# Kernel tuning notes

Hardware: AMD Instinct MI355X
Metric: run time of the kernel (lower is better)

## Reference

```python
import jax, jax.numpy as jnp
import numpy as np

N_NODES = 50000
N_EDGES = 800000
D_IN = 64
D_OUT = 64


def setup_inputs() -> dict:
    key = jax.random.key(0)
    ks = jax.random.split(key, 5)
    feat = jax.random.normal(ks[0], (N_NODES, D_IN), dtype=jnp.float32)
    src = jax.random.randint(ks[1], (N_EDGES,), 0, N_NODES, dtype=jnp.int64)
    dst = jax.random.randint(ks[2], (N_EDGES,), 0, N_NODES, dtype=jnp.int64)
    # Xavier-uniform-ish scale for weights
    lim = float(np.sqrt(6.0 / (D_IN + D_OUT)) * np.sqrt(2.0))
    W_neigh = jax.random.uniform(ks[3], (D_OUT, D_IN), dtype=jnp.float32, minval=-lim, maxval=lim)
    W_self = jax.random.uniform(ks[4], (D_OUT, D_IN), dtype=jnp.float32, minval=-lim, maxval=lim)
    b_self = jnp.zeros((D_OUT,), dtype=jnp.float32)
    return {"feat": feat, "src": src, "dst": dst,
            "W_neigh": W_neigh, "W_self": W_self, "b_self": b_self}


def reference(feat, src, dst, W_neigh, W_self, b_self):
    # srcdata = fc_neigh(feat_src)  -> [N, D_OUT]
    srcdata = feat @ W_neigh.T
    # A_div.T @ srcdata == mean of transformed source feats over in-edges per dst.
    # deg[j] = A.sum(0)[j]; column scaling by 1/deg then transpose-SpMM.
    agg = jax.ops.segment_sum(srcdata[src], dst, num_segments=N_NODES)  # [N, D_OUT]
    deg = jax.ops.segment_sum(jnp.ones_like(dst, dtype=srcdata.dtype), dst,
                              num_segments=N_NODES)  # [N]
    # Zero-degree columns stay zero in the sparse product (no stored nonzeros).
    dstdata = jnp.where(deg[:, None] > 0, agg / jnp.maximum(deg, 1.0)[:, None], 0.0)
    # rst = fc_self(feat_dst) + dstdata ; feat_dst = feat[:N_dst] = feat (square A)
    return feat @ W_self.T + b_self + dstdata
```

## Files before the change

### kernel.cpp

```cpp
#include <hip/hip_runtime.h>

#define N_NODES 50000
#define N_EDGES 800000
#define D 64
#define RB 128
#define NBUCK 391
#define NFEATBLK 3125
#define GN 64
#define NCHUNK 196
#define CHUNK 4096
#define SUBCAP 40
#define SCAP 3072
#define ALD 68

typedef __attribute__((ext_vector_type(8))) __bf16 bf16x8;
typedef __attribute__((ext_vector_type(4))) float f32x4;
typedef __attribute__((ext_vector_type(2))) float f32x2;

__device__ inline unsigned f2bf(float f) {
    unsigned b = __builtin_bit_cast(unsigned, f);
    b += 0x7fffu + ((b >> 16) & 1u);
    return b >> 16;
}

__device__ inline void acc16(float* acc, uint4 v) {
    f32x2 a;
    a = __builtin_amdgcn_cvt_pk_f32_fp8((int)v.x, false); acc[0]  += a.x; acc[1]  += a.y;
    a = __builtin_amdgcn_cvt_pk_f32_fp8((int)v.x, true);  acc[2]  += a.x; acc[3]  += a.y;
    a = __builtin_amdgcn_cvt_pk_f32_fp8((int)v.y, false); acc[4]  += a.x; acc[5]  += a.y;
    a = __builtin_amdgcn_cvt_pk_f32_fp8((int)v.y, true);  acc[6]  += a.x; acc[7]  += a.y;
    a = __builtin_amdgcn_cvt_pk_f32_fp8((int)v.z, false); acc[8]  += a.x; acc[9]  += a.y;
    a = __builtin_amdgcn_cvt_pk_f32_fp8((int)v.z, true);  acc[10] += a.x; acc[11] += a.y;
    a = __builtin_amdgcn_cvt_pk_f32_fp8((int)v.w, false); acc[12] += a.x; acc[13] += a.y;
    a = __builtin_amdgcn_cvt_pk_f32_fp8((int)v.w, true);  acc[14] += a.x; acc[15] += a.y;
}

__global__ __launch_bounds__(256) void prep_scatter_kernel(
        const float* __restrict__ feat, const float* __restrict__ Wn, const float* __restrict__ Ws,
        const int* __restrict__ src, const int* __restrict__ dst,
        unsigned* __restrict__ fq,
        unsigned short* __restrict__ wnb, unsigned short* __restrict__ wsb,
        unsigned int* __restrict__ ebuf, unsigned char* __restrict__ cntArr) {
    __shared__ int cntB[NBUCK];
    int b = blockIdx.x;
    int t = threadIdx.x;
    if (b < NCHUNK) {
        for (int i = t; i < NBUCK; i += 256) cntB[i] = 0;
        __syncthreads();
        int e0 = b * CHUNK;
#pragma unroll
        for (int k = 0; k < 16; ++k) {
            int e = e0 + k * 256 + t;
            if (e < N_EDGES) {
                int dv = dst[e];
                int bk = dv >> 7;
                int slot = atomicAdd(&cntB[bk], 1);
                if (slot < SUBCAP)
                    ebuf[((size_t)bk * NCHUNK + b) * SUBCAP + slot] =
                        (unsigned)src[e] | ((unsigned)(dv & (RB - 1)) << 16);
            }
        }
        __syncthreads();
        for (int i = t; i < NBUCK; i += 256) {
            int c = cntB[i];
            cntArr[(size_t)b * NBUCK + i] = (unsigned char)(c < SUBCAP ? c : SUBCAP);
        }
    } else if (b < NCHUNK + NFEATBLK) {
        int i = (b - NCHUNK) * 256 + t;
        float4 v = ((const float4*)feat)[i];
        int q = __builtin_amdgcn_cvt_pk_fp8_f32(v.x, v.y, 0, false);
        q = __builtin_amdgcn_cvt_pk_fp8_f32(v.z, v.w, q, true);
        fq[i] = (unsigned)q;
    } else {
        for (int i = t; i < D * D; i += 256) {
            wnb[i] = (unsigned short)f2bf(Wn[i]);
            wsb[i] = (unsigned short)f2bf(Ws[i]);
        }
    }
}

__global__ __launch_bounds__(256) void gather_mfma_kernel(
        const float* __restrict__ feat, const unsigned char* __restrict__ fq,
        const unsigned int* __restrict__ ebuf, const unsigned char* __restrict__ cntArr,
        const unsigned short* __restrict__ wsb, const unsigned short* __restrict__ wnb,
        const float* __restrict__ bias, float* __restrict__ out) {
    __shared__ int cnt[RB];
    __shared__ int cur[RB];
    __shared__ unsigned short sorted[SCAP];
    __shared__ float agg[GN * ALD];
    int t = threadIdx.x;
    int bk = blockIdx.x >> 1;
    int half = blockIdx.x & 1;
    if (t < RB) cnt[t] = 0;
    __syncthreads();
    int cc = 0;
    const unsigned int* slab = ebuf + ((size_t)bk * NCHUNK + t) * SUBCAP;
    if (t < NCHUNK) cc = cntArr[(size_t)t * NBUCK + bk];
    for (int j = 0; j < cc; j += 4) {
        uint4 v = *(const uint4*)(slab + j);
        atomicAdd(&cnt[(v.x >> 16) & (RB - 1)], 1);
        if (j + 1 < cc) atomicAdd(&cnt[(v.y >> 16) & (RB - 1)], 1);
        if (j + 2 < cc) atomicAdd(&cnt[(v.z >> 16) & (RB - 1)], 1);
        if (j + 3 < cc) atomicAdd(&cnt[(v.w >> 16) & (RB - 1)], 1);
    }
    __syncthreads();
    int c = (t < RB) ? cnt[t] : 0;
    if (t < RB) cur[t] = c;
    __syncthreads();
    for (int d = 1; d < RB; d <<= 1) {
        int v = (t < RB && t >= d) ? cur[t - d] : 0;
        __syncthreads();
        if (t < RB) cur[t] += v;
        __syncthreads();
    }
    if (t < RB) cur[t] -= c;
    __syncthreads();
    for (int j = 0; j < cc; j += 4) {
        uint4 v = *(const uint4*)(slab + j);
        int p;
        p = atomicAdd(&cur[(v.x >> 16) & (RB - 1)], 1);
        if (p < SCAP) sorted[p] = (unsigned short)(v.x & 0xFFFFu);
        if (j + 1 < cc) { p = atomicAdd(&cur[(v.y >> 16) & (RB - 1)], 1); if (p < SCAP) sorted[p] = (unsigned short)(v.y & 0xFFFFu); }
        if (j + 2 < cc) { p = atomicAdd(&cur[(v.z >> 16) & (RB - 1)], 1); if (p < SCAP) sorted[p] = (unsigned short)(v.z & 0xFFFFu); }
        if (j + 3 < cc) { p = atomicAdd(&cur[(v.w >> 16) & (RB - 1)], 1); if (p < SCAP) sorted[p] = (unsigned short)(v.w & 0xFFFFu); }
    }
    __syncthreads();
    int ns = t >> 2, p = t & 3;
    int dl = half * GN + ns;
    int dg = cnt[dl];
    int start = cur[dl] - dg;
    float acc[16];
#pragma unroll
    for (int j = 0; j < 16; ++j) acc[j] = 0.f;
    const unsigned char* fqp = fq + p * 16;
    int i = 0;
    for (; i + 4 <= dg; i += 4) {
        int id0 = sorted[start + i + 0];
        int id1 = sorted[start + i + 1];
        int id2 = sorted[start + i + 2];
        int id3 = sorted[start + i + 3];
        uint4 v0 = *(const uint4*)(fqp + (size_t)id0 * D);
        uint4 v1 = *(const uint4*)(fqp + (size_t)id1 * D);
        uint4 v2 = *(const uint4*)(fqp + (size_t)id2 * D);
        uint4 v3 = *(const uint4*)(fqp + (size_t)id3 * D);
        acc16(acc, v0); acc16(acc, v1); acc16(acc, v2); acc16(acc, v3);
    }
    for (; i < dg; ++i) {
        int id = sorted[start + i];
        uint4 v = *(const uint4*)(fqp + (size_t)id * D);
        acc16(acc, v);
    }
    float inv = (dg > 0) ? 1.0f / (float)dg : 0.f;
#pragma unroll
    for (int j = 0; j < 16; j += 4) {
        float4 o = make_float4(acc[j] * inv, acc[j + 1] * inv, acc[j + 2] * inv, acc[j + 3] * inv);
        *(float4*)(&agg[ns * ALD + p * 16 + j]) = o;
    }
    __syncthreads();
    int r0 = blockIdx.x * GN;
    int w = t >> 6, lane = t & 63;
    int m = lane & 15, quad = lane >> 4;
    int row = r0 + 16 * w + m;
    int rowA = row < N_NODES ? row : N_NODES - 1;
    const float* fr = feat + (size_t)rowA * D + quad * 8;
    float4 f0 = *(const float4*)(fr + 0);
    float4 f1 = *(const float4*)(fr + 4);
    float4 f2 = *(const float4*)(fr + 32);
    float4 f3 = *(const float4*)(fr + 36);
    bf16x8 aS0, aS1, aA0, aA1;
    aS0[0] = (__bf16)f0.x; aS0[1] = (__bf16)f0.y; aS0[2] = (__bf16)f0.z; aS0[3] = (__bf16)f0.w;
    aS0[4] = (__bf16)f1.x; aS0[5] = (__bf16)f1.y; aS0[6] = (__bf16)f1.z; aS0[7] = (__bf16)f1.w;
    aS1[0] = (__bf16)f2.x; aS1[1] = (__bf16)f2.y; aS1[2] = (__bf16)f2.z; aS1[3] = (__bf16)f2.w;
    aS1[4] = (__bf16)f3.x; aS1[5] = (__bf16)f3.y; aS1[6] = (__bf16)f3.z; aS1[7] = (__bf16)f3.w;
#pragma unroll
    for (int j = 0; j < 8; ++j) {
        aA0[j] = (__bf16)agg[(16 * w + m) * ALD + 0  + quad * 8 + j];
        aA1[j] = (__bf16)agg[(16 * w + m) * ALD + 32 + quad * 8 + j];
    }
#pragma unroll
    for (int tt = 0; tt < 4; ++tt) {
        int nn = 16 * tt + m;
        bf16x8 bS0 = *(const bf16x8*)(wsb + (size_t)nn * D + 0  + quad * 8);
        bf16x8 bS1 = *(const bf16x8*)(wsb + (size_t)nn * D + 32 + quad * 8);
        bf16x8 bN0 = *(const bf16x8*)(wnb + (size_t)nn * D + 0  + quad * 8);
        bf16x8 bN1 = *(const bf16x8*)(wnb + (size_t)nn * D + 32 + quad * 8);
        f32x4 cc4 = {0.f, 0.f, 0.f, 0.f};
        cc4 = __builtin_amdgcn_mfma_f32_16x16x32_bf16(aS0, bS0, cc4, 0, 0, 0);
        cc4 = __builtin_amdgcn_mfma_f32_16x16x32_bf16(aS1, bS1, cc4, 0, 0, 0);
        cc4 = __builtin_amdgcn_mfma_f32_16x16x32_bf16(aA0, bN0, cc4, 0, 0, 0);
        cc4 = __builtin_amdgcn_mfma_f32_16x16x32_bf16(aA1, bN1, cc4, 0, 0, 0);
        float bv = bias[16 * tt + m];
#pragma unroll
        for (int reg = 0; reg < 4; ++reg) {
            int orow = r0 + 16 * w + quad * 4 + reg;
            if (orow < N_NODES)
                out[(size_t)orow * D + 16 * tt + m] = cc4[reg] + bv;
        }
    }
}

extern "C" void kernel_launch(void* const* d_in, const int* in_sizes, int n_in,
                              void* d_out, int out_size, void* d_ws, size_t ws_size,
                              hipStream_t stream) {
    const float* feat  = (const float*)d_in[0];
    const int*   src   = (const int*)d_in[1];
    const int*   dst   = (const int*)d_in[2];
    const float* Wn    = (const float*)d_in[3];
    const float* Wself = (const float*)d_in[4];
    const float* bself = (const float*)d_in[5];
    float* out = (float*)d_out;

    unsigned*       featq = (unsigned*)d_ws;
    unsigned short* wnb   = (unsigned short*)(featq + (size_t)N_NODES * D / 4);
    unsigned short* wsb   = wnb + D * D;
    unsigned int*   ebuf  = (unsigned int*)(wsb + D * D);
    unsigned char*  cntArr = (unsigned char*)(ebuf + (size_t)NBUCK * NCHUNK * SUBCAP);

    prep_scatter_kernel<<<NCHUNK + NFEATBLK + 1, 256, 0, stream>>>(
        feat, Wn, Wself, src, dst, featq, wnb, wsb, ebuf, cntArr);
    gather_mfma_kernel<<<2 * NBUCK, 256, 0, stream>>>(
        feat, (const unsigned char*)featq, ebuf, cntArr, wsb, wnb, bself, out);
}
```

Measured before the change: 114.1 us.

## Split gather blocks into quarter-buckets and two-way split each node's edge list

The gather kernel now launches four blocks per 128-node bucket instead of two, with each block handling 32 destination nodes. Each node's in-edge list is split between two thread groups whose partial sums are added and scaled by 1/deg when building the MFMA operand. The output tile per wave is reduced to 16 rows by two column tiles. The aim is more parallelism and more memory-level concurrency in the latency-bound gather, at the cost of every block re-reading its bucket's full edge slab and filtering it, which quadruples that redundant work instead of doubling it.

```diff
diff --git a/kernel.cpp b/kernel.cpp
--- a/kernel.cpp
+++ b/kernel.cpp
@@ -6,11 +6,12 @@
 #define RB 128
 #define NBUCK 391
 #define NFEATBLK 3125
-#define GN 64
+#define GN 32
+#define NGB (4 * NBUCK)
 #define NCHUNK 196
 #define CHUNK 4096
 #define SUBCAP 40
-#define SCAP 3072
+#define QCAP 768
 #define ALD 68
 
 typedef __attribute__((ext_vector_type(8))) __bf16 bf16x8;
@@ -84,57 +85,60 @@
         const unsigned int* __restrict__ ebuf, const unsigned char* __restrict__ cntArr,
         const unsigned short* __restrict__ wsb, const unsigned short* __restrict__ wnb,
         const float* __restrict__ bias, float* __restrict__ out) {
-    __shared__ int cnt[RB];
-    __shared__ int cur[RB];
-    __shared__ unsigned short sorted[SCAP];
-    __shared__ float agg[GN * ALD];
+    __shared__ int cnt[GN];
+    __shared__ int cur[GN];
+    __shared__ unsigned short sorted[QCAP];
+    __shared__ float agg[2 * GN * ALD];
+    __shared__ float invA[GN];
     int t = threadIdx.x;
-    int bk = blockIdx.x >> 1;
-    int half = blockIdx.x & 1;
-    if (t < RB) cnt[t] = 0;
+    int bk = blockIdx.x >> 2;
+    int qtr = blockIdx.x & 3;
+    if (t < GN) cnt[t] = 0;
     __syncthreads();
     int cc = 0;
     const unsigned int* slab = ebuf + ((size_t)bk * NCHUNK + t) * SUBCAP;
     if (t < NCHUNK) cc = cntArr[(size_t)t * NBUCK + bk];
     for (int j = 0; j < cc; j += 4) {
         uint4 v = *(const uint4*)(slab + j);
-        atomicAdd(&cnt[(v.x >> 16) & (RB - 1)], 1);
-        if (j + 1 < cc) atomicAdd(&cnt[(v.y >> 16) & (RB - 1)], 1);
-        if (j + 2 < cc) atomicAdd(&cnt[(v.z >> 16) & (RB - 1)], 1);
-        if (j + 3 < cc) atomicAdd(&cnt[(v.w >> 16) & (RB - 1)], 1);
-    }
-    __syncthreads();
-    int c = (t < RB) ? cnt[t] : 0;
-    if (t < RB) cur[t] = c;
-    __syncthreads();
-    for (int d = 1; d < RB; d <<= 1) {
-        int v = (t < RB && t >= d) ? cur[t - d] : 0;
-        __syncthreads();
-        if (t < RB) cur[t] += v;
-        __syncthreads();
-    }
-    if (t < RB) cur[t] -= c;
+        int dl;
+        dl = (int)(v.x >> 16); if ((dl >> 5) == qtr) atomicAdd(&cnt[dl & 31], 1);
+        if (j + 1 < cc) { dl = (int)(v.y >> 16); if ((dl >> 5) == qtr) atomicAdd(&cnt[dl & 31], 1); }
+        if (j + 2 < cc) { dl = (int)(v.z >> 16); if ((dl >> 5) == qtr) atomicAdd(&cnt[dl & 31], 1); }
+        if (j + 3 < cc) { dl = (int)(v.w >> 16); if ((dl >> 5) == qtr) atomicAdd(&cnt[dl & 31], 1); }
+    }
+    __syncthreads();
+    int c = (t < GN) ? cnt[t] : 0;
+    if (t < GN) cur[t] = c;
+    __syncthreads();
+    for (int d = 1; d < GN; d <<= 1) {
+        int v = (t < GN && t >= d) ? cur[t - d] : 0;
+        __syncthreads();
+        if (t < GN) cur[t] += v;
+        __syncthreads();
+    }
+    if (t < GN) cur[t] -= c;
     __syncthreads();
     for (int j = 0; j < cc; j += 4) {
         uint4 v = *(const uint4*)(slab + j);
-        int p;
-        p = atomicAdd(&cur[(v.x >> 16) & (RB - 1)], 1);
-        if (p < SCAP) sorted[p] = (unsigned short)(v.x & 0xFFFFu);
-        if (j + 1 < cc) { p = atomicAdd(&cur[(v.y >> 16) & (RB - 1)], 1); if (p < SCAP) sorted[p] = (unsigned short)(v.y & 0xFFFFu); }
-        if (j + 2 < cc) { p = atomicAdd(&cur[(v.z >> 16) & (RB - 1)], 1); if (p < SCAP) sorted[p] = (unsigned short)(v.z & 0xFFFFu); }
-        if (j + 3 < cc) { p = atomicAdd(&cur[(v.w >> 16) & (RB - 1)], 1); if (p < SCAP) sorted[p] = (unsigned short)(v.w & 0xFFFFu); }
-    }
-    __syncthreads();
-    int ns = t >> 2, p = t & 3;
-    int dl = half * GN + ns;
-    int dg = cnt[dl];
-    int start = cur[dl] - dg;
+        int dl, p;
+        dl = (int)(v.x >> 16);
+        if ((dl >> 5) == qtr) { p = atomicAdd(&cur[dl & 31], 1); if (p < QCAP) sorted[p] = (unsigned short)(v.x & 0xFFFFu); }
+        if (j + 1 < cc) { dl = (int)(v.y >> 16); if ((dl >> 5) == qtr) { p = atomicAdd(&cur[dl & 31], 1); if (p < QCAP) sorted[p] = (unsigned short)(v.y & 0xFFFFu); } }
+        if (j + 2 < cc) { dl = (int)(v.z >> 16); if ((dl >> 5) == qtr) { p = atomicAdd(&cur[dl & 31], 1); if (p < QCAP) sorted[p] = (unsigned short)(v.z & 0xFFFFu); } }
+        if (j + 3 < cc) { dl = (int)(v.w >> 16); if ((dl >> 5) == qtr) { p = atomicAdd(&cur[dl & 31], 1); if (p < QCAP) sorted[p] = (unsigned short)(v.w & 0xFFFFu); } }
+    }
+    __syncthreads();
+    int ns = t >> 3, g = (t >> 2) & 1, p = t & 3;
+    int dg = cnt[ns];
+    int start = cur[ns] - dg;
+    int h = (dg + 1) >> 1;
+    int lo = g ? h : 0, hi = g ? dg : h;
     float acc[16];
 #pragma unroll
     for (int j = 0; j < 16; ++j) acc[j] = 0.f;
     const unsigned char* fqp = fq + p * 16;
-    int i = 0;
-    for (; i + 4 <= dg; i += 4) {
+    int i = lo;
+    for (; i + 4 <= hi; i += 4) {
         int id0 = sorted[start + i + 0];
         int id1 = sorted[start + i + 1];
         int id2 = sorted[start + i + 2];
@@ -145,22 +149,24 @@
         uint4 v3 = *(const uint4*)(fqp + (size_t)id3 * D);
         acc16(acc, v0); acc16(acc, v1); acc16(acc, v2); acc16(acc, v3);
     }
-    for (; i < dg; ++i) {
+    for (; i < hi; ++i) {
         int id = sorted[start + i];
         uint4 v = *(const uint4*)(fqp + (size_t)id * D);
         acc16(acc, v);
     }
-    float inv = (dg > 0) ? 1.0f / (float)dg : 0.f;
 #pragma unroll
     for (int j = 0; j < 16; j += 4) {
-        float4 o = make_float4(acc[j] * inv, acc[j + 1] * inv, acc[j + 2] * inv, acc[j + 3] * inv);
-        *(float4*)(&agg[ns * ALD + p * 16 + j]) = o;
-    }
+        *(float4*)(&agg[(ns * 2 + g) * ALD + p * 16 + j]) =
+            make_float4(acc[j], acc[j + 1], acc[j + 2], acc[j + 3]);
+    }
+    if (g == 0 && p == 0) invA[ns] = (dg > 0) ? 1.0f / (float)dg : 0.f;
     __syncthreads();
     int r0 = blockIdx.x * GN;
     int w = t >> 6, lane = t & 63;
     int m = lane & 15, quad = lane >> 4;
-    int row = r0 + 16 * w + m;
+    int rt = w & 1;
+    int nr = rt * 16 + m;
+    int row = r0 + nr;
     int rowA = row < N_NODES ? row : N_NODES - 1;
     const float* fr = feat + (size_t)rowA * D + quad * 8;
     float4 f0 = *(const float4*)(fr + 0);
@@ -172,14 +178,19 @@
     aS0[4] = (__bf16)f1.x; aS0[5] = (__bf16)f1.y; aS0[6] = (__bf16)f1.z; aS0[7] = (__bf16)f1.w;
     aS1[0] = (__bf16)f2.x; aS1[1] = (__bf16)f2.y; aS1[2] = (__bf16)f2.z; aS1[3] = (__bf16)f2.w;
     aS1[4] = (__bf16)f3.x; aS1[5] = (__bf16)f3.y; aS1[6] = (__bf16)f3.z; aS1[7] = (__bf16)f3.w;
+    float iv = invA[nr];
 #pragma unroll
     for (int j = 0; j < 8; ++j) {
-        aA0[j] = (__bf16)agg[(16 * w + m) * ALD + 0  + quad * 8 + j];
-        aA1[j] = (__bf16)agg[(16 * w + m) * ALD + 32 + quad * 8 + j];
-    }
-#pragma unroll
-    for (int tt = 0; tt < 4; ++tt) {
-        int nn = 16 * tt + m;
+        int b0 = (nr * 2) * ALD + quad * 8 + j;
+        int b1 = (nr * 2 + 1) * ALD + quad * 8 + j;
+        aA0[j] = (__bf16)((agg[b0] + agg[b1]) * iv);
+        aA1[j] = (__bf16)((agg[b0 + 32] + agg[b1 + 32]) * iv);
+    }
+    int ct0 = (w >> 1) * 2;
+#pragma unroll
+    for (int cti = 0; cti < 2; ++cti) {
+        int ct = ct0 + cti;
+        int nn = 16 * ct + m;
         bf16x8 bS0 = *(const bf16x8*)(wsb + (size_t)nn * D + 0  + quad * 8);
         bf16x8 bS1 = *(const bf16x8*)(wsb + (size_t)nn * D + 32 + quad * 8);
         bf16x8 bN0 = *(const bf16x8*)(wnb + (size_t)nn * D + 0  + quad * 8);
@@ -189,12 +200,12 @@
         cc4 = __builtin_amdgcn_mfma_f32_16x16x32_bf16(aS1, bS1, cc4, 0, 0, 0);
         cc4 = __builtin_amdgcn_mfma_f32_16x16x32_bf16(aA0, bN0, cc4, 0, 0, 0);
         cc4 = __builtin_amdgcn_mfma_f32_16x16x32_bf16(aA1, bN1, cc4, 0, 0, 0);
-        float bv = bias[16 * tt + m];
+        float bv = bias[16 * ct + m];
 #pragma unroll
         for (int reg = 0; reg < 4; ++reg) {
-            int orow = r0 + 16 * w + quad * 4 + reg;
+            int orow = r0 + rt * 16 + quad * 4 + reg;
             if (orow < N_NODES)
-                out[(size_t)orow * D + 16 * tt + m] = cc4[reg] + bv;
+                out[(size_t)orow * D + 16 * ct + m] = cc4[reg] + bv;
         }
     }
 }
@@ -218,6 +229,6 @@
 
     prep_scatter_kernel<<<NCHUNK + NFEATBLK + 1, 256, 0, stream>>>(
         feat, Wn, Wself, src, dst, featq, wnb, wsb, ebuf, cntArr);
-    gather_mfma_kernel<<<2 * NBUCK, 256, 0, stream>>>(
+    gather_mfma_kernel<<<NGB, 256, 0, stream>>>(
         feat, (const unsigned char*)featq, ebuf, cntArr, wsb, wnb, bself, out);
 }
```

Result: slower. 125.9 us (+10.4%).
